# Kernel tuning notes

Hardware: AMD Instinct MI355X
Metric: run time of the kernel (lower is better)

Reference implementation:

```python
import jax, jax.numpy as jnp
import numpy as np

B, S, D = 4, 2048, 1024
H = 16
HD = D // H  # 64


def setup_inputs() -> dict:
    key = jax.random.key(0)
    ks = jax.random.split(key, 8)
    scale = 1.0 / np.sqrt(D)
    return {
        "hidden_states": jax.random.normal(ks[0], (B, S, D), dtype=jnp.float32),
        "attention_mask": jnp.ones((B, 1, 1, S), dtype=jnp.int32),
        "Wq": jax.random.normal(ks[1], (D, D), dtype=jnp.float32) * scale,
        "bq": jax.random.normal(ks[2], (D,), dtype=jnp.float32) * 0.02,
        "Wk": jax.random.normal(ks[3], (D, D), dtype=jnp.float32) * scale,
        "bk": jax.random.normal(ks[4], (D,), dtype=jnp.float32) * 0.02,
        "Wv": jax.random.normal(ks[5], (D, D), dtype=jnp.float32) * scale,
        "bv": jax.random.normal(ks[6], (D,), dtype=jnp.float32) * 0.02,
    }


def _split_heads(x):
    # [b, t, (h d)] -> [b, h, t, d]
    b, t, _ = x.shape
    return x.reshape(b, t, H, HD).transpose(0, 2, 1, 3)


def reference(hidden_states, attention_mask, Wq, bq, Wk, bk, Wv, bv):
    # Linear projections (torch Linear: x @ W.T + b)
    q = _split_heads(hidden_states @ Wq.T + bq)
    k = _split_heads(hidden_states @ Wk.T + bk)
    v = _split_heads(hidden_states @ Wv.T + bv)

    # scaled dot-product scores: [b, h, s, s]
    scores = jnp.einsum("bhqd,bhkd->bhqk", q, k) / np.sqrt(HD)

    s = scores.shape[-1]
    causal = jnp.tril(jnp.ones((s, s), dtype=bool))[None, None]
    neg_inf = jnp.float32(-jnp.inf)
    scores = jnp.where(causal, scores, neg_inf)
    # attention_mask is 0/1 keep mask: [b, 1, 1, s]
    scores = jnp.where(attention_mask == 0, neg_inf, scores)

    probs = jax.nn.softmax(scores, axis=-1)  # dropout p=0 (eval)
    ctx = jnp.einsum("bhqk,bhkd->bhqd", probs, v)
    # [b, h, t, d] -> [b, t, h*d]
    return ctx.transpose(0, 2, 1, 3).reshape(hidden_states.shape[0], s, D)
```

## Files before the change

### kernel.cpp

```cpp
#include <hip/hip_runtime.h>
#include <hip/hip_bf16.h>
#include <math.h>


#define B_ 4
#define S_ 2048
#define D_ 1024
#define H_ 16
#define HD_ 64
#define M_ (B_ * S_)

typedef unsigned short u16;
typedef unsigned int u32;
typedef __attribute__((ext_vector_type(4))) float f32x4;
typedef __attribute__((ext_vector_type(8))) short bf16x8;

__device__ __forceinline__ u16 f2bfu_rn(float x) {
    u32 u = __builtin_bit_cast(u32, x);
    return (u16)((u + 0x8000u) >> 16);
}

__device__ __forceinline__ u32 pack_bf16(float lo, float hi) {
    u32 a = __builtin_bit_cast(u32, lo) + 0x8000u;
    u32 b = __builtin_bit_cast(u32, hi) + 0x8000u;
    return __builtin_amdgcn_perm(b, a, 0x07060302u);
}

__device__ __forceinline__ void gl2lds16(const void* g, void* l) {
    __builtin_amdgcn_global_load_lds(
        (const __attribute__((address_space(1))) u32*)g,
        (__attribute__((address_space(3))) u32*)l, 16, 0, 0);
}

#define XN  8388608u
#define WN  1048576u
__global__ __launch_bounds__(256) void convert_bf16(
    const float* __restrict__ X,  const float* __restrict__ Wq,
    const float* __restrict__ Wk, const float* __restrict__ Wv,
    u16* __restrict__ Xb, u16* __restrict__ Wqb,
    u16* __restrict__ Wkb, u16* __restrict__ Wvb)
{
    size_t idx = ((size_t)blockIdx.x * 256 + threadIdx.x) * 8;
    const float* src; u16* dst; size_t off;
    if (idx < XN)                { src = X;  dst = Xb;  off = idx; }
    else if (idx < XN + WN)      { src = Wq; dst = Wqb; off = idx - XN; }
    else if (idx < XN + 2 * WN)  { src = Wk; dst = Wkb; off = idx - XN - WN; }
    else                         { src = Wv; dst = Wvb; off = idx - XN - 2 * WN; }
    float4 a = *(const float4*)(src + off);
    float4 b = *(const float4*)(src + off + 4);
    uint4 o;
    o.x = (u32)f2bfu_rn(a.x) | ((u32)f2bfu_rn(a.y) << 16);
    o.y = (u32)f2bfu_rn(a.z) | ((u32)f2bfu_rn(a.w) << 16);
    o.z = (u32)f2bfu_rn(b.x) | ((u32)f2bfu_rn(b.y) << 16);
    o.w = (u32)f2bfu_rn(b.z) | ((u32)f2bfu_rn(b.w) << 16);
    *(uint4*)(dst + off) = o;
}

#define QSCALE 0.18033688011112042f

__global__ __launch_bounds__(256) void qkv_mfma8(
    const u16* __restrict__ Xb,
    const u16* __restrict__ Wqb, const u16* __restrict__ Wkb,
    const u16* __restrict__ Wvb,
    const float* __restrict__ bq, const float* __restrict__ bk,
    const float* __restrict__ bv,
    u16* __restrict__ Qb, u16* __restrict__ Kb, u16* __restrict__ Vtb)
{
    const int which = blockIdx.y;
    const int bxl = ((blockIdx.x & 7) << 6) | (blockIdx.x >> 3);

    const u16* Asrc; const u16* Bsrc; const float* bias; u16* Out;
    int m0, n0;
    if (which == 0)      { Asrc = Xb;  Bsrc = Wqb; bias = bq; Out = Qb;
                           m0 = (bxl >> 3) * 128; n0 = (bxl & 7) * 128; }
    else if (which == 1) { Asrc = Xb;  Bsrc = Wkb; bias = bk; Out = Kb;
                           m0 = (bxl >> 3) * 128; n0 = (bxl & 7) * 128; }
    else                 { Asrc = Wvb; Bsrc = Xb;  bias = bv; Out = Vtb;
                           m0 = (bxl & 7) * 128; n0 = (bxl >> 3) * 128; }

    __shared__ u16 As[3][128][32];
    __shared__ u16 Bs[3][128][32];

    const int t = threadIdx.x;
    const int wave = t >> 6, lane = t & 63;
    const int qd = lane >> 4, l15 = lane & 15;
    const int wm = wave >> 1, wn = wave & 1;

    auto STAGE_A = [&](int tt, int u) {
        const int buf = tt % 3, k0 = tt * 32;
        const int rb = wave * 32 + u * 16;
        const int r  = rb + (lane >> 2);
        const int g  = (lane & 3) ^ ((r >> 1) & 3);
        gl2lds16(Asrc + (size_t)(m0 + r) * D_ + k0 + g * 8, &As[buf][rb][0]);
    };
    auto STAGE_B = [&](int tt, int u) {
        const int buf = tt % 3, k0 = tt * 32;
        const int rb = wave * 32 + u * 16;
        const int r  = rb + (lane >> 2);
        const int g  = (lane & 3) ^ ((r >> 1) & 3);
        gl2lds16(Bsrc + (size_t)(n0 + r) * D_ + k0 + g * 8, &Bs[buf][rb][0]);
    };

    const f32x4 zero = {0.f, 0.f, 0.f, 0.f};
    f32x4 acc[4][4];
#pragma unroll
    for (int i = 0; i < 4; ++i)
#pragma unroll
        for (int j = 0; j < 4; ++j) acc[i][j] = zero;

    STAGE_A(0, 0); STAGE_A(0, 1); STAGE_B(0, 0); STAGE_B(0, 1);
    STAGE_A(1, 0); STAGE_A(1, 1); STAGE_B(1, 0); STAGE_B(1, 1);
    asm volatile("s_waitcnt vmcnt(4)" ::: "memory");
    __builtin_amdgcn_s_barrier();

    for (int tt = 0; tt < 32; ++tt) {
        const int buf = tt % 3;

        bf16x8 af[4], bfv[4];
#pragma unroll
        for (int nt = 0; nt < 4; ++nt) {
            const int row = wn * 64 + nt * 16 + l15;
            bfv[nt] = *(const bf16x8*)&Bs[buf][row][(qd ^ ((row >> 1) & 3)) * 8];
        }
#pragma unroll
        for (int mt = 0; mt < 4; ++mt) {
            const int row = wm * 64 + mt * 16 + l15;
            af[mt] = *(const bf16x8*)&As[buf][row][(qd ^ ((row >> 1) & 3)) * 8];
        }
        if (tt <= 29) {
            const int t2 = tt + 2;
            STAGE_A(t2, 0); STAGE_A(t2, 1); STAGE_B(t2, 0); STAGE_B(t2, 1);
        }
        asm volatile("s_waitcnt lgkmcnt(0)" ::: "memory");
        __builtin_amdgcn_sched_barrier(0);
        __builtin_amdgcn_s_setprio(1);
#pragma unroll
        for (int mt = 0; mt < 4; ++mt)
#pragma unroll
            for (int nt = 0; nt < 4; ++nt)
                acc[mt][nt] = __builtin_amdgcn_mfma_f32_16x16x32_bf16(
                    af[mt], bfv[nt], acc[mt][nt], 0, 0, 0);
        __builtin_amdgcn_s_setprio(0);
        if (tt <= 28) asm volatile("s_waitcnt vmcnt(4)" ::: "memory");
        else          asm volatile("s_waitcnt vmcnt(0)" ::: "memory");
        __builtin_amdgcn_s_barrier();
    }

    if (which < 2) {
#pragma unroll
        for (int nt = 0; nt < 4; ++nt) {
            int n = n0 + wn * 64 + nt * 16 + l15;
            float bv_ = bias[n];
            int h = n >> 6, hd = n & 63;
#pragma unroll
            for (int mt = 0; mt < 4; ++mt)
#pragma unroll
                for (int r = 0; r < 4; ++r) {
                    int m = m0 + wm * 64 + mt * 16 + qd * 4 + r;
                    int bb = m >> 11, s = m & 2047;
                    float v = acc[mt][nt][r] + bv_;
                    if (which == 0) v *= QSCALE;
                    Out[(((size_t)(bb * H_ + h)) * S_ + s) * HD_ + hd] = f2bfu_rn(v);
                }
        }
    } else {
#pragma unroll
        for (int mt = 0; mt < 4; ++mt)
#pragma unroll
            for (int r = 0; r < 4; ++r) {
                int f = m0 + wm * 64 + mt * 16 + qd * 4 + r;
                float bv_ = bias[f];
                int h = f >> 6, hd = f & 63;
#pragma unroll
                for (int nt = 0; nt < 4; ++nt) {
                    int tok = n0 + wn * 64 + nt * 16 + l15;
                    int bb = tok >> 11, s = tok & 2047;
                    float v = acc[mt][nt][r] + bv_;
                    Out[(((size_t)(bb * H_ + h)) * HD_ + hd) * S_ + s] = f2bfu_rn(v);
                }
            }
    }
}

__global__ __launch_bounds__(256) void attn_chunk(
    const u16* __restrict__ Qb, const u16* __restrict__ Kb,
    const u16* __restrict__ Vtb, const int* __restrict__ amask,
    float* __restrict__ Oout, float* __restrict__ Opart,
    float* __restrict__ L0, float* __restrict__ L1)
{
    const int bid = blockIdx.x;
    const int rank = bid >> 6;
    int x;
    if (rank < 17)      x = rank;
    else if (rank == 17) x = 32;
    else {
        int i = (rank - 18) >> 1;
        x = ((rank - 18) & 1) ? (33 + i) : (17 + i);
    }
    const int bh  = ((bid & 7) << 3) | ((bid >> 3) & 7);
    const int b = bh >> 4, h = bh & 15;
    int qt, jt0, jt1; bool second;
    if (x < 32) { qt = 31 - x; jt0 = 0;  jt1 = min(qt, 15); second = false; }
    else        { qt = 63 - x; jt0 = 16; jt1 = qt;          second = true;  }
    const int q0 = qt * 64;

    const int t = threadIdx.x;
    const int wave = t >> 6, lane = t & 63;
    const int qd = lane >> 4, l15 = lane & 15;

    __shared__ u16 Ks[64][64];
    __shared__ u16 Vts[64][64];
    __shared__ u16 Ps[64][72];

    const size_t base = (size_t)bh * S_ * HD_;
    const u16* Qg = Qb + base;
    const u16* Kg = Kb + base;
    const u16* Vg = Vtb + base;
    const int* am = amask + b * S_;

    bf16x8 qf[2];
    {
        const u16* qrow = Qg + (size_t)(q0 + wave * 16 + l15) * HD_;
        qf[0] = *(const bf16x8*)(qrow + qd * 8);
        qf[1] = *(const bf16x8*)(qrow + 32 + qd * 8);
    }
    bf16x8 onesf;
    {
        short v = (l15 == 0) ? (short)0x3F80 : (short)0;
        onesf = (bf16x8){v, v, v, v, v, v, v, v};
    }

    const f32x4 zero = {0.f, 0.f, 0.f, 0.f};
    f32x4 o[5];
#pragma unroll
    for (int i = 0; i < 5; ++i) o[i] = zero;

    const int qloc = wave * 16 + l15;
    u32* prow32 = (u32*)&Ps[qloc][0];

    auto ISSUE_K = [&](int jt) {
        const int j0 = jt * 64;
#pragma unroll
        for (int i = 0; i < 2; ++i) {
            int r0  = (wave * 2 + i) * 8;
            int row = r0 + (lane >> 3);
            int g   = (lane & 7) ^ (row & 7);
            gl2lds16(Kg + (size_t)(j0 + row) * HD_ + g * 8, &Ks[r0][0]);
        }
    };
    auto ISSUE_V = [&](int jt) {
        const int j0 = jt * 64;
#pragma unroll
        for (int i = 0; i < 2; ++i) {
            int r0  = (wave * 2 + i) * 8;
            int row = r0 + (lane >> 3);
            int g   = (lane & 7) ^ (row & 7);
            gl2lds16(Vg + (size_t)row * S_ + j0 + g * 8, &Vts[r0][0]);
        }
    };

    int am0, am1, am2, am3;
    auto PROBE = [&](int jt) {
        const int j0 = jt * 64;
        am0 = am[j0 + l15];      am1 = am[j0 + 16 + l15];
        am2 = am[j0 + 32 + l15]; am3 = am[j0 + 48 + l15];
    };

    ISSUE_K(jt0);
    ISSUE_V(jt0);
    PROBE(jt0);
    __syncthreads();

    for (int jt = jt0; jt <= jt1; ++jt) {
        const int j0 = jt * 64;

        f32x4 sacc[4];
#pragma unroll
        for (int nt = 0; nt < 4; ++nt) sacc[nt] = zero;
        __builtin_amdgcn_s_setprio(1);
#pragma unroll
        for (int ks = 0; ks < 2; ++ks) {
#pragma unroll
            for (int nt = 0; nt < 4; ++nt) {
                int arow = nt * 16 + l15;
                int ap = (ks * 4 + qd) ^ (arow & 7);
                bf16x8 kf = *(const bf16x8*)&Ks[arow][ap * 8];
                sacc[nt] = __builtin_amdgcn_mfma_f32_16x16x32_bf16(
                    kf, qf[ks], sacc[nt], 0, 0, 0);
            }
        }
        __builtin_amdgcn_s_setprio(0);

        __syncthreads();
        if (jt < jt1) ISSUE_K(jt + 1);

        const bool fast = __all((int)((am0 != 0) & (am1 != 0) &
                                      (am2 != 0) & (am3 != 0)));
        const bool diag = (jt == qt);
#pragma unroll
        for (int nt = 0; nt < 4; ++nt) {
            float p[4];
#pragma unroll
            for (int r = 0; r < 4; ++r) {
                int kl = nt * 16 + qd * 4 + r;
                float s = sacc[nt][r];
                if (!fast) {
                    if (am[j0 + kl] == 0) s = -1e30f;
                }
                if (diag && kl > qloc) s = -1e30f;
                p[r] = __builtin_amdgcn_exp2f(s);
            }
            uint2 w;
            w.x = pack_bf16(p[0], p[1]);
            w.y = pack_bf16(p[2], p[3]);
            *(uint2*)&prow32[nt * 8 + qd * 2] = w;
        }

        __builtin_amdgcn_s_setprio(1);
#pragma unroll
        for (int ks = 0; ks < 2; ++ks) {
            int arow = wave * 16 + l15;
            bf16x8 pf = *(const bf16x8*)&Ps[arow][ks * 32 + qd * 8];
#pragma unroll
            for (int nt = 0; nt < 4; ++nt) {
                int brow = nt * 16 + l15;
                int bp = (ks * 4 + qd) ^ (brow & 7);
                bf16x8 vf = *(const bf16x8*)&Vts[brow][bp * 8];
                o[nt] = __builtin_amdgcn_mfma_f32_16x16x32_bf16(
                    pf, vf, o[nt], 0, 0, 0);
            }
            o[4] = __builtin_amdgcn_mfma_f32_16x16x32_bf16(
                pf, onesf, o[4], 0, 0, 0);
        }
        __builtin_amdgcn_s_setprio(0);

        if (jt < jt1) {
            __syncthreads();
            ISSUE_V(jt + 1);
            PROBE(jt + 1);
        }
    }

    if (!second) {
        if (qt <= 15) {
#pragma unroll
            for (int r = 0; r < 4; ++r) {
                float l = __shfl(o[4][r], lane & 48);
                float inv = 1.0f / l;
                int q = q0 + wave * 16 + qd * 4 + r;
                float* op = Oout + ((size_t)(b * S_ + q)) * D_ + h * HD_;
#pragma unroll
                for (int nt = 0; nt < 4; ++nt)
                    op[nt * 16 + l15] = o[nt][r] * inv;
            }
        } else {
#pragma unroll
            for (int r = 0; r < 4; ++r) {
                int q = q0 + wave * 16 + qd * 4 + r;
                float* op = Oout + ((size_t)(b * S_ + q)) * D_ + h * HD_;
#pragma unroll
                for (int nt = 0; nt < 4; ++nt)
                    op[nt * 16 + l15] = o[nt][r];
                if (l15 == 0) L0[(size_t)bh * S_ + q] = o[4][r];
            }
        }
    } else {
#pragma unroll
        for (int r = 0; r < 4; ++r) {
            int q = q0 + wave * 16 + qd * 4 + r;
            int sh = q - 1024;
            float* op = Opart + ((size_t)bh * 1024 + sh) * HD_;
#pragma unroll
            for (int nt = 0; nt < 4; ++nt)
                op[nt * 16 + l15] = o[nt][r];
            if (l15 == 0) L1[(size_t)bh * 1024 + sh] = o[4][r];
        }
    }
}

__global__ __launch_bounds__(256) void combine(
    float* __restrict__ out, const float* __restrict__ Opart,
    const float* __restrict__ L0, const float* __restrict__ L1)
{
    size_t i = ((size_t)blockIdx.x * 256 + threadIdx.x) * 4;
    int d  = (int)(i & (D_ - 1));
    int bs = (int)(i >> 10);
    int b  = bs >> 10, sh = bs & 1023;
    int s  = sh + 1024;
    int h  = d >> 6;
    int bh = b * H_ + h;
    float l = L0[(size_t)bh * S_ + s] + L1[(size_t)bh * 1024 + sh];
    float inv = 1.0f / l;
    float* op = out + ((size_t)(b * S_ + s)) * D_ + d;
    const float* pp = Opart + ((size_t)bh * 1024 + sh) * HD_ + (d & 63);
    float4 v = *(float4*)op;
    float4 p = *(const float4*)pp;
    v.x = (v.x + p.x) * inv; v.y = (v.y + p.y) * inv;
    v.z = (v.z + p.z) * inv; v.w = (v.w + p.w) * inv;
    *(float4*)op = v;
}

extern "C" void kernel_launch(void* const* d_in, const int* in_sizes, int n_in,
                              void* d_out, int out_size, void* d_ws, size_t ws_size,
                              hipStream_t stream) {
    (void)in_sizes; (void)n_in; (void)out_size; (void)ws_size;
    const float* X    = (const float*)d_in[0];
    const int*   mask = (const int*)d_in[1];
    const float* Wq   = (const float*)d_in[2];
    const float* bq   = (const float*)d_in[3];
    const float* Wk   = (const float*)d_in[4];
    const float* bk   = (const float*)d_in[5];
    const float* Wv   = (const float*)d_in[6];
    const float* bv   = (const float*)d_in[7];
    float* out = (float*)d_out;

    u16* Xb  = (u16*)d_ws;
    u16* Wqb = Xb  + XN;
    u16* Wkb = Wqb + WN;
    u16* Wvb = Wkb + WN;
    u16* Qb  = Wvb + WN;
    u16* Kb  = Qb  + XN;
    u16* Vtb = Kb  + XN;
    float* Opart = (float*)(Vtb + XN);
    float* L0 = Opart + (size_t)64 * 1024 * 64;
    float* L1 = L0 + (size_t)64 * 2048;

    convert_bf16<<<(XN + 3 * WN) / (256 * 8), 256, 0, stream>>>(
        X, Wq, Wk, Wv, Xb, Wqb, Wkb, Wvb);
    qkv_mfma8<<<dim3(512, 3), 256, 0, stream>>>(
        Xb, Wqb, Wkb, Wvb, bq, bk, bv, Qb, Kb, Vtb);
    attn_chunk<<<dim3(3072), 256, 0, stream>>>(
        Qb, Kb, Vtb, mask, out, Opart, L0, L1);
    combine<<<(B_ * 1024 * D_ / 4) / 256, 256, 0, stream>>>(out, Opart, L0, L1);
}
```

Before: 231.2 us.

## Fuse Q and K projections to share X tiles; split V projection kernel

```diff
diff --git a/kernel.cpp b/kernel.cpp
--- a/kernel.cpp
+++ b/kernel.cpp
@@ -58,28 +58,19 @@
 
 #define QSCALE 0.18033688011112042f
 
-__global__ __launch_bounds__(256) void qkv_mfma8(
+__global__ __launch_bounds__(256) void qkv_qk(
     const u16* __restrict__ Xb,
     const u16* __restrict__ Wqb, const u16* __restrict__ Wkb,
-    const u16* __restrict__ Wvb,
     const float* __restrict__ bq, const float* __restrict__ bk,
-    const float* __restrict__ bv,
-    u16* __restrict__ Qb, u16* __restrict__ Kb, u16* __restrict__ Vtb)
+    u16* __restrict__ Qb, u16* __restrict__ Kb)
 {
-    const int which = blockIdx.y;
     const int bxl = ((blockIdx.x & 7) << 6) | (blockIdx.x >> 3);
-
-    const u16* Asrc; const u16* Bsrc; const float* bias; u16* Out;
-    int m0, n0;
-    if (which == 0)      { Asrc = Xb;  Bsrc = Wqb; bias = bq; Out = Qb;
-                           m0 = (bxl >> 3) * 128; n0 = (bxl & 7) * 128; }
-    else if (which == 1) { Asrc = Xb;  Bsrc = Wkb; bias = bk; Out = Kb;
-                           m0 = (bxl >> 3) * 128; n0 = (bxl & 7) * 128; }
-    else                 { Asrc = Wvb; Bsrc = Xb;  bias = bv; Out = Vtb;
-                           m0 = (bxl & 7) * 128; n0 = (bxl >> 3) * 128; }
+    const int m0 = (bxl >> 3) * 128;
+    const int n0 = (bxl & 7) * 128;
 
     __shared__ u16 As[3][128][32];
-    __shared__ u16 Bs[3][128][32];
+    __shared__ u16 Bq[3][128][32];
+    __shared__ u16 Bk[3][128][32];
 
     const int t = threadIdx.x;
     const int wave = t >> 6, lane = t & 63;
@@ -91,14 +82,124 @@
         const int rb = wave * 32 + u * 16;
         const int r  = rb + (lane >> 2);
         const int g  = (lane & 3) ^ ((r >> 1) & 3);
-        gl2lds16(Asrc + (size_t)(m0 + r) * D_ + k0 + g * 8, &As[buf][rb][0]);
+        gl2lds16(Xb + (size_t)(m0 + r) * D_ + k0 + g * 8, &As[buf][rb][0]);
+    };
+    auto STAGE_Q = [&](int tt, int u) {
+        const int buf = tt % 3, k0 = tt * 32;
+        const int rb = wave * 32 + u * 16;
+        const int r  = rb + (lane >> 2);
+        const int g  = (lane & 3) ^ ((r >> 1) & 3);
+        gl2lds16(Wqb + (size_t)(n0 + r) * D_ + k0 + g * 8, &Bq[buf][rb][0]);
+    };
+    auto STAGE_K = [&](int tt, int u) {
+        const int buf = tt % 3, k0 = tt * 32;
+        const int rb = wave * 32 + u * 16;
+        const int r  = rb + (lane >> 2);
+        const int g  = (lane & 3) ^ ((r >> 1) & 3);
+        gl2lds16(Wkb + (size_t)(n0 + r) * D_ + k0 + g * 8, &Bk[buf][rb][0]);
+    };
+
+    const f32x4 zero = {0.f, 0.f, 0.f, 0.f};
+    f32x4 aq[4][4], ak[4][4];
+#pragma unroll
+    for (int i = 0; i < 4; ++i)
+#pragma unroll
+        for (int j = 0; j < 4; ++j) { aq[i][j] = zero; ak[i][j] = zero; }
+
+    STAGE_A(0, 0); STAGE_A(0, 1); STAGE_Q(0, 0); STAGE_Q(0, 1);
+    STAGE_K(0, 0); STAGE_K(0, 1);
+    STAGE_A(1, 0); STAGE_A(1, 1); STAGE_Q(1, 0); STAGE_Q(1, 1);
+    STAGE_K(1, 0); STAGE_K(1, 1);
+    asm volatile("s_waitcnt vmcnt(6)" ::: "memory");
+    __builtin_amdgcn_s_barrier();
+
+    for (int tt = 0; tt < 32; ++tt) {
+        const int buf = tt % 3;
+
+        bf16x8 af[4], bqf[4], bkf[4];
+#pragma unroll
+        for (int mt = 0; mt < 4; ++mt) {
+            const int row = wm * 64 + mt * 16 + l15;
+            af[mt] = *(const bf16x8*)&As[buf][row][(qd ^ ((row >> 1) & 3)) * 8];
+        }
+#pragma unroll
+        for (int nt = 0; nt < 4; ++nt) {
+            const int row = wn * 64 + nt * 16 + l15;
+            const int p = (qd ^ ((row >> 1) & 3)) * 8;
+            bqf[nt] = *(const bf16x8*)&Bq[buf][row][p];
+            bkf[nt] = *(const bf16x8*)&Bk[buf][row][p];
+        }
+        if (tt <= 29) {
+            const int t2 = tt + 2;
+            STAGE_A(t2, 0); STAGE_A(t2, 1);
+            STAGE_Q(t2, 0); STAGE_Q(t2, 1);
+            STAGE_K(t2, 0); STAGE_K(t2, 1);
+        }
+        asm volatile("s_waitcnt lgkmcnt(0)" ::: "memory");
+        __builtin_amdgcn_sched_barrier(0);
+        __builtin_amdgcn_s_setprio(1);
+#pragma unroll
+        for (int mt = 0; mt < 4; ++mt)
+#pragma unroll
+            for (int nt = 0; nt < 4; ++nt) {
+                aq[mt][nt] = __builtin_amdgcn_mfma_f32_16x16x32_bf16(
+                    af[mt], bqf[nt], aq[mt][nt], 0, 0, 0);
+                ak[mt][nt] = __builtin_amdgcn_mfma_f32_16x16x32_bf16(
+                    af[mt], bkf[nt], ak[mt][nt], 0, 0, 0);
+            }
+        __builtin_amdgcn_s_setprio(0);
+        if (tt <= 28) asm volatile("s_waitcnt vmcnt(6)" ::: "memory");
+        else          asm volatile("s_waitcnt vmcnt(0)" ::: "memory");
+        __builtin_amdgcn_s_barrier();
+    }
+
+#pragma unroll
+    for (int nt = 0; nt < 4; ++nt) {
+        int n = n0 + wn * 64 + nt * 16 + l15;
+        float bq_ = bq[n], bk_ = bk[n];
+        int h = n >> 6, hd = n & 63;
+#pragma unroll
+        for (int mt = 0; mt < 4; ++mt)
+#pragma unroll
+            for (int r = 0; r < 4; ++r) {
+                int m = m0 + wm * 64 + mt * 16 + qd * 4 + r;
+                int bb = m >> 11, s = m & 2047;
+                size_t oi = (((size_t)(bb * H_ + h)) * S_ + s) * HD_ + hd;
+                Qb[oi] = f2bfu_rn((aq[mt][nt][r] + bq_) * QSCALE);
+                Kb[oi] = f2bfu_rn(ak[mt][nt][r] + bk_);
+            }
+    }
+}
+
+__global__ __launch_bounds__(256) void qkv_v(
+    const u16* __restrict__ Xb, const u16* __restrict__ Wvb,
+    const float* __restrict__ bv, u16* __restrict__ Vtb)
+{
+    const int bxl = ((blockIdx.x & 7) << 6) | (blockIdx.x >> 3);
+    const int m0 = (bxl & 7) * 128;
+    const int n0 = (bxl >> 3) * 128;
+
+    __shared__ u16 As[3][128][32];
+    __shared__ u16 Bs[3][128][32];
+
+    const int t = threadIdx.x;
+    const int wave = t >> 6, lane = t & 63;
+    const int qd = lane >> 4, l15 = lane & 15;
+    const int wm = wave >> 1, wn = wave & 1;
+
+    auto STAGE_A = [&](int tt, int u) {
+        const int buf = tt % 3, k0 = tt * 32;
+        const int rb = wave * 32 + u * 16;
+        const int r  = rb + (lane >> 2);
+        const int g  = (lane & 3) ^ ((r >> 1) & 3);
+        gl2lds16(Wvb + (size_t)(m0 + r) * D_ + k0 + g * 8, &As[buf][rb][0]);
     };
     auto STAGE_B = [&](int tt, int u) {
         const int buf = tt % 3, k0 = tt * 32;
         const int rb = wave * 32 + u * 16;
         const int r  = rb + (lane >> 2);
         const int g  = (lane & 3) ^ ((r >> 1) & 3);
-        gl2lds16(Bsrc + (size_t)(n0 + r) * D_ + k0 + g * 8, &Bs[buf][rb][0]);
+        gl2lds16(Xb + (size_t)(n0 + r) * D_ + k0 + g * 8, &Bs[buf][rb][0]);
     };
 
     const f32x4 zero = {0.f, 0.f, 0.f, 0.f};
@@ -146,40 +247,21 @@
         __builtin_amdgcn_s_barrier();
     }
 
-    if (which < 2) {
-#pragma unroll
-        for (int nt = 0; nt < 4; ++nt) {
-            int n = n0 + wn * 64 + nt * 16 + l15;
-            float bv_ = bias[n];
-            int h = n >> 6, hd = n & 63;
-#pragma unroll
-            for (int mt = 0; mt < 4; ++mt)
-#pragma unroll
-                for (int r = 0; r < 4; ++r) {
-                    int m = m0 + wm * 64 + mt * 16 + qd * 4 + r;
-                    int bb = m >> 11, s = m & 2047;
-                    float v = acc[mt][nt][r] + bv_;
-                    if (which == 0) v *= QSCALE;
-                    Out[(((size_t)(bb * H_ + h)) * S_ + s) * HD_ + hd] = f2bfu_rn(v);
-                }
-        }
-    } else {
-#pragma unroll
-        for (int mt = 0; mt < 4; ++mt)
-#pragma unroll
-            for (int r = 0; r < 4; ++r) {
-                int f = m0 + wm * 64 + mt * 16 + qd * 4 + r;
-                float bv_ = bias[f];
-                int h = f >> 6, hd = f & 63;
-#pragma unroll
-                for (int nt = 0; nt < 4; ++nt) {
-                    int tok = n0 + wn * 64 + nt * 16 + l15;
-                    int bb = tok >> 11, s = tok & 2047;
-                    float v = acc[mt][nt][r] + bv_;
-                    Out[(((size_t)(bb * H_ + h)) * HD_ + hd) * S_ + s] = f2bfu_rn(v);
-                }
-            }
-    }
+#pragma unroll
+    for (int mt = 0; mt < 4; ++mt)
+#pragma unroll
+        for (int r = 0; r < 4; ++r) {
+            int f = m0 + wm * 64 + mt * 16 + qd * 4 + r;
+            float bv_ = bv[f];
+            int h = f >> 6, hd = f & 63;
+#pragma unroll
+            for (int nt = 0; nt < 4; ++nt) {
+                int tok = n0 + wn * 64 + nt * 16 + l15;
+                int bb = tok >> 11, s = tok & 2047;
+                float v = acc[mt][nt][r] + bv_;
+                Vtb[(((size_t)(bb * H_ + h)) * HD_ + hd) * S_ + s] = f2bfu_rn(v);
+            }
+        }
 }
 
 __global__ __launch_bounds__(256) void attn_chunk(
@@ -210,7 +292,7 @@
 
     __shared__ u16 Ks[64][64];
     __shared__ u16 Vts[64][64];
-    __shared__ u16 Ps[64][72];
+    __shared__ u16 Ps[64][76];
 
     const size_t base = (size_t)bh * S_ * HD_;
     const u16* Qg = Qb + base;
@@ -427,8 +509,10 @@
 
     convert_bf16<<<(XN + 3 * WN) / (256 * 8), 256, 0, stream>>>(
         X, Wq, Wk, Wv, Xb, Wqb, Wkb, Wvb);
-    qkv_mfma8<<<dim3(512, 3), 256, 0, stream>>>(
-        Xb, Wqb, Wkb, Wvb, bq, bk, bv, Qb, Kb, Vtb);
+    qkv_qk<<<dim3(512), 256, 0, stream>>>(
+        Xb, Wqb, Wkb, bq, bk, Qb, Kb);
+    qkv_v<<<dim3(512), 256, 0, stream>>>(
+        Xb, Wvb, bv, Vtb);
     attn_chunk<<<dim3(3072), 256, 0, stream>>>(
         Qb, Kb, Vtb, mask, out, Opart, L0, L1);
     combine<<<(B_ * 1024 * D_ / 4) / 256, 256, 0, stream>>>(out, Opart, L0, L1);
```

Measured after the change: 243.6 us. 1.05x slower.
